# Kernel optimization log

Hardware: AMD Instinct MI355X
Metric: run time of the kernel (lower is better)

The kernel has to match this reference:

```python
import jax, jax.numpy as jnp
import numpy as np

NUM_HEADS = 32
NUM_KV_HEADS = 8
HEAD_DIM = 128
N_REP = NUM_HEADS // NUM_KV_HEADS
ROPE_BASE = 10000.0
NEG_INF = -3.4e38  # large negative for causal mask (matches fp32 min magnitude behavior)


def setup_inputs() -> dict:
    key = jax.random.key(0)
    ks = jax.random.split(key, 5)
    B, S, D = 1, 2048, 4096
    KV = NUM_KV_HEADS * HEAD_DIM  # 1024
    scale = 0.02
    return {
        "hidden_states": jax.random.normal(ks[0], (B, S, D), dtype=jnp.float32),
        "Wq": jax.random.normal(ks[1], (D, D), dtype=jnp.float32) * scale,
        "Wk": jax.random.normal(ks[2], (D, KV), dtype=jnp.float32) * scale,
        "Wv": jax.random.normal(ks[3], (D, KV), dtype=jnp.float32) * scale,
        "Wo": jax.random.normal(ks[4], (D, D), dtype=jnp.float32) * scale,
    }


def _rotate_half(x):
    x1, x2 = jnp.split(x, 2, axis=-1)
    return jnp.concatenate((-x2, x1), axis=-1)


def _rope_cos_sin(B, S, dtype):
    # Qwen/Llama-style rotary embedding, base 10000, position_ids = arange(S)
    inv_freq = 1.0 / (ROPE_BASE ** (jnp.arange(0, HEAD_DIM, 2, dtype=jnp.float32) / HEAD_DIM))
    pos = jnp.arange(S, dtype=jnp.float32)[None, :]            # [1, S] (broadcast over batch)
    freqs = pos[..., None] * inv_freq[None, None, :]           # [1, S, D/2]
    emb = jnp.concatenate((freqs, freqs), axis=-1)             # [1, S, D]
    return jnp.cos(emb).astype(dtype), jnp.sin(emb).astype(dtype)


def reference(hidden_states, Wq, Wk, Wv, Wo):
    B, S, D = hidden_states.shape
    dtype = hidden_states.dtype

    q = (hidden_states @ Wq).reshape(B, S, NUM_HEADS, HEAD_DIM).transpose(0, 2, 1, 3)      # [B,H,S,d]
    k = (hidden_states @ Wk).reshape(B, S, NUM_KV_HEADS, HEAD_DIM).transpose(0, 2, 1, 3)   # [B,Hkv,S,d]
    v = (hidden_states @ Wv).reshape(B, S, NUM_KV_HEADS, HEAD_DIM).transpose(0, 2, 1, 3)

    cos, sin = _rope_cos_sin(B, S, dtype)
    cos = cos[:, None, :, :]  # unsqueeze head dim
    sin = sin[:, None, :, :]
    q = q * cos + _rotate_half(q) * sin
    k = k * cos + _rotate_half(k) * sin

    # repeat_kv: [B,Hkv,S,d] -> [B,H,S,d]
    k = jnp.repeat(k, N_REP, axis=1)
    v = jnp.repeat(v, N_REP, axis=1)

    attn = jnp.einsum("bhqd,bhkd->bhqk", q, k) / jnp.sqrt(jnp.asarray(HEAD_DIM, dtype))
    causal = jnp.where(jnp.arange(S)[:, None] >= jnp.arange(S)[None, :], 0.0, NEG_INF).astype(dtype)
    attn = attn + causal[None, None, :, :]
    attn = jax.nn.softmax(attn.astype(jnp.float32), axis=-1).astype(dtype)

    out = jnp.einsum("bhqk,bhkd->bhqd", attn, v)           # [B,H,S,d]
    out = out.transpose(0, 2, 1, 3).reshape(B, S, NUM_HEADS * HEAD_DIM)
    return out @ Wo
```

## Files before the change

kernel.cpp:

```cpp
#include <hip/hip_runtime.h>
#include <stdint.h>

typedef float f32x4 __attribute__((ext_vector_type(4)));
typedef __bf16 bf16x8 __attribute__((ext_vector_type(8)));
typedef unsigned short u16;
typedef unsigned short u16x8 __attribute__((ext_vector_type(8)));

__device__ __forceinline__ u16 f2b(float f) {
    union { float f; unsigned u; } v; v.f = f;
    return (u16)((v.u + 0x7fffu + ((v.u >> 16) & 1u)) >> 16);
}
__device__ __forceinline__ float b2f(u16 b) {
    union { unsigned u; float f; } v; v.u = ((unsigned)b) << 16;
    return v.f;
}

__device__ __forceinline__ void gload16(const u16* g, u16* s) {
    __builtin_amdgcn_global_load_lds((const __attribute__((address_space(1))) void*)g,
                                     (__attribute__((address_space(3))) void*)s, 16, 0, 0);
}

__global__ __launch_bounds__(256) void k_cast(const float* __restrict__ src, u16* __restrict__ dst, int n) {
    int i = (blockIdx.x * 256 + threadIdx.x) * 8;
    if (i >= n) return;
    const float4* s = (const float4*)(src + i);
    float4 a = s[0], b = s[1];
    u16x8 o;
    o[0] = f2b(a.x); o[1] = f2b(a.y); o[2] = f2b(a.z); o[3] = f2b(a.w);
    o[4] = f2b(b.x); o[5] = f2b(b.y); o[6] = f2b(b.z); o[7] = f2b(b.w);
    *(u16x8*)(dst + i) = o;
}

__global__ __launch_bounds__(256) void k_transpose(const float* __restrict__ src, u16* __restrict__ dst,
                                                   int R, int C) {
    __shared__ float tile[64][65];
    int c0 = blockIdx.x * 64, r0 = blockIdx.y * 64;
    int tx = threadIdx.x & 63, ty = threadIdx.x >> 6;
    #pragma unroll
    for (int r = ty; r < 64; r += 4)
        tile[r][tx] = src[(size_t)(r0 + r) * C + (c0 + tx)];
    __syncthreads();
    #pragma unroll
    for (int r = ty; r < 64; r += 4)
        dst[(size_t)(c0 + r) * R + (r0 + tx)] = f2b(tile[tx][r]);
}

__global__ __launch_bounds__(256) void k_vt(const u16* __restrict__ QKV, u16* __restrict__ VT) {
    __shared__ u16 tile[64][66];
    int kh = blockIdx.z;
    int s0 = blockIdx.y * 64;
    int d0 = blockIdx.x * 64;
    int tx = threadIdx.x & 63, ty = threadIdx.x >> 6;
    #pragma unroll
    for (int r = ty; r < 64; r += 4)
        tile[r][tx] = QKV[(size_t)(s0 + r) * 6144 + 5120 + kh * 128 + d0 + tx];
    __syncthreads();
    #pragma unroll
    for (int r = ty; r < 64; r += 4)
        VT[(size_t)kh * 262144 + (size_t)(d0 + r) * 2048 + s0 + tx] = tile[tx][r];
}

#define STAGE_A(h) do { \
    _Pragma("unroll") for (int i_ = 0; i_ < MFR / 4; ++i_) \
        gload16(gA + (size_t)((h) * (MFR * 16) + i_ * 8) * K + kn, &Ah[nb][h][w * (MFR * 2) + i_ * 8][0]); \
} while (0)
#define STAGE_B1(h) gload16(gB + (size_t)((h) * 64) * K + kn, &Bh[nb][h][w * 8][0])
#define STAGE_ALL do { \
    _Pragma("unroll") for (int h_ = 0; h_ < 2; ++h_) STAGE_A(h_); \
    _Pragma("unroll") for (int h_ = 0; h_ < NFR; ++h_) STAGE_B1(h_); } while (0)
#define RD_AF(MH, AF) do { \
    _Pragma("unroll") for (int mm = 0; mm < MFR / 2; ++mm) \
    _Pragma("unroll") for (int x = 0; x < 2; ++x) \
        AF[mm][x] = *(const bf16x8*)&Ah[c][wm][((MH) * (MFR / 2) + mm) * 16 + lr][(x * 32 + lk) ^ swz]; } while (0)
#define RD_BF1(NF) do { \
    int bc_ = wn * (NFR * 16) + (NF) * 16; \
    _Pragma("unroll") for (int x = 0; x < 2; ++x) \
        bfr[NF][x] = *(const bf16x8*)&Bh[c][bc_ >> 6][(bc_ & 63) + lr][(x * 32 + lk) ^ swz]; } while (0)
#define MMAH(MH, NF, AF) do { \
    _Pragma("unroll") for (int x = 0; x < 2; ++x) \
    _Pragma("unroll") for (int mm = 0; mm < MFR / 2; ++mm) \
        acc[(MH) * (MFR / 2) + mm][NF] = __builtin_amdgcn_mfma_f32_16x16x32_bf16( \
            AF[mm][x], bfr[NF][x], acc[(MH) * (MFR / 2) + mm][NF], 0, 0, 0); } while (0)

template <int MFR, int NFR, typename OutT>
__device__ __forceinline__ void gemm_core(const u16* __restrict__ A, const u16* __restrict__ Bt,
                                          OutT* __restrict__ C, int K, int ldc, int m0, int n0) {
    __shared__ u16 Ah[2][2][MFR * 16][64];
    __shared__ u16 Bh[2][NFR][64][64];
    constexpr int LPT = MFR / 2 + NFR;
    int tid = threadIdx.x;
    int l = tid & 63, w = tid >> 6;
    int wm = w >> 2, wn = w & 3;
    int lr = l & 15, lg = l >> 4, lk = lg * 8;
    int swz = (lr & 7) << 3;
    int srow8 = l >> 3;
    int scol = ((l & 7) ^ srow8) * 8;
    const u16* gA = A  + (size_t)(m0 + w * (MFR * 2) + srow8) * K + scol;
    const u16* gB = Bt + (size_t)(n0 + w * 8 + srow8) * K + scol;
    f32x4 acc[MFR][NFR] = {};
    int NT = K >> 6;

    {
        int kn = 0, nb = 0;
        STAGE_ALL;
    }

    #pragma unroll 2
    for (int t = 0; t < NT; ++t) {
        int c = t & 1, nb = c ^ 1;
        int kn = (t + 1) << 6;
        bool last = (t == NT - 1);
        bf16x8 af0[MFR / 2][2], af1[MFR / 2][2], bfr[NFR][2];
        if (!last) {
            STAGE_ALL;
            asm volatile("s_waitcnt vmcnt(%0)" :: "n"(LPT) : "memory");
        } else {
            asm volatile("s_waitcnt vmcnt(0)" ::: "memory");
        }
        __builtin_amdgcn_s_barrier();
        RD_AF(0, af0);
        #pragma unroll
        for (int nf = 0; nf < NFR; ++nf) {
            RD_BF1(nf);
            __builtin_amdgcn_s_setprio(1);
            MMAH(0, nf, af0);
            __builtin_amdgcn_s_setprio(0);
        }
        RD_AF(1, af1);
        __builtin_amdgcn_s_setprio(1);
        #pragma unroll
        for (int nf = 0; nf < NFR; ++nf)
            MMAH(1, nf, af1);
        __builtin_amdgcn_s_setprio(0);
        __builtin_amdgcn_s_barrier();
    }

    #pragma unroll
    for (int m = 0; m < MFR; ++m)
        #pragma unroll
        for (int n = 0; n < NFR; ++n)
            #pragma unroll
            for (int e = 0; e < 4; ++e) {
                int row = m0 + wm * (MFR * 16) + m * 16 + lg * 4 + e;
                int col = n0 + wn * (NFR * 16) + n * 16 + lr;
                if constexpr (sizeof(OutT) == 4)
                    C[(size_t)row * ldc + col] = acc[m][n][e];
                else
                    C[(size_t)row * ldc + col] = f2b(acc[m][n][e]);
            }
}

__global__ __launch_bounds__(512, 2) void k_gemm_qkv(const u16* __restrict__ hsb,
        const u16* __restrict__ WqkvT, u16* __restrict__ QKVb) {
    int bid = blockIdx.x;
    int ord = (bid & 7) * 32 + (bid >> 3);
    int mt = ord >> 5, nt = ord & 31;
    gemm_core<8, 3, u16>(hsb, WqkvT, QKVb, 4096, 6144, mt * 256, nt * 192);
}

__global__ __launch_bounds__(512, 2) void k_gemm_out(const u16* __restrict__ Ob, const u16* __restrict__ WoT,
                                                     float* __restrict__ out) {
    int bid = blockIdx.x;
    int ord = (bid & 7) * 32 + (bid >> 3);
    int mt = ord >> 4, nt = ord & 15;
    gemm_core<4, 4, float>(Ob, WoT, out, 4096, 4096, mt * 128, nt * 256);
}

__global__ __launch_bounds__(256) void k_rope(u16* __restrict__ QKV) {
    int t = blockIdx.x * 256 + threadIdx.x;
    int i = t & 63;
    int rest = t >> 6;
    int head = rest % 40;
    int s = rest / 40;
    if (s >= 2048) return;
    u16* base = (head < 32) ? (QKV + (size_t)s * 6144 + head * 128)
                            : (QKV + (size_t)s * 6144 + 4096 + (head - 32) * 128);
    float inv = exp2f((float)i * (-13.287712379549449f / 64.0f));
    float fr = (float)s * inv;
    float sn, cs;
    sincosf(fr, &sn, &cs);
    float x1 = b2f(base[i]), x2 = b2f(base[i + 64]);
    base[i]      = f2b(x1 * cs - x2 * sn);
    base[i + 64] = f2b(x2 * cs + x1 * sn);
}

__global__ __launch_bounds__(256, 2) void k_attn(const u16* __restrict__ QKV,
                                                 const u16* __restrict__ VT, u16* __restrict__ O) {
    __shared__ u16 Kl[2][64][128];
    __shared__ u16 VTl[128][64];
    __shared__ u16 Pl[4][32][68];
    int bid = blockIdx.x;
    int kh = bid & 7;
    int x = bid >> 3;
    int j = x >> 2;
    int h = kh * 4 + (x & 3);
    int qb = (j < 8) ? j : 23 - j;
    int q0 = qb * 128;
    int t = threadIdx.x, l = t & 63, w = t >> 6;
    int lr = l & 15, lg = l >> 4;
    const float cexp = 0.12751742f;
    const u16* Kh = QKV + 4096 + kh * 128;
    const u16* VTh = VT + (size_t)kh * 262144;

#define ATT_STAGE_K(B, KV0) do { \
    _Pragma("unroll") for (int i_ = 0; i_ < 4; ++i_) { \
        int r0_ = w * 16 + i_ * 4; \
        int row_ = r0_ + (l >> 4); \
        gload16(Kh + (size_t)((KV0) + row_) * 6144 + ((l & 15) ^ (row_ & 7)) * 8, \
                &Kl[B][r0_][0]); \
    } } while (0)
#define ATT_STAGE_V(KV0) do { \
    _Pragma("unroll") for (int i_ = 0; i_ < 4; ++i_) { \
        int r0_ = w * 32 + i_ * 8; \
        int row_ = r0_ + (l >> 3); \
        gload16(VTh + (size_t)row_ * 2048 + (KV0) + ((l & 7) ^ (row_ & 7)) * 8, \
                &VTl[r0_][0]); \
    } } while (0)

    bf16x8 qf[2][4];
    #pragma unroll
    for (int rb = 0; rb < 2; ++rb) {
        size_t qoff = (size_t)(q0 + w * 32 + rb * 16 + lr) * 6144 + h * 128 + lg * 8;
        #pragma unroll
        for (int d = 0; d < 4; ++d)
            qf[rb][d] = *(const bf16x8*)(QKV + qoff + d * 32);
    }
    bf16x8 ones;
    #pragma unroll
    for (int i = 0; i < 8; ++i) ones[i] = (__bf16)1.0f;

    f32x4 oacc[2][8] = {};
    f32x4 osum[2] = {};
    float mrow[2][4];
    #pragma unroll
    for (int rb = 0; rb < 2; ++rb)
        #pragma unroll
        for (int e = 0; e < 4; ++e) mrow[rb][e] = -3.0e38f;

    int ntiles = 2 * qb + 2;
    int rowmax = q0 + w * 32 + 31;

    ATT_STAGE_K(0, 0);

    for (int kt = 0; kt < ntiles; ++kt) {
        int ck = kt & 1;
        int kv0 = kt * 64;
        bool compute = (kv0 <= rowmax);
        bool more = (kt + 1 < ntiles);
        asm volatile("s_waitcnt vmcnt(0)" ::: "memory");
        __builtin_amdgcn_s_barrier();
        ATT_STAGE_V(kv0);
        if (more) ATT_STAGE_K(ck ^ 1, kv0 + 64);
        __builtin_amdgcn_sched_barrier(0);

        f32x4 sacc[2][4] = {};
        if (compute) {
            #pragma unroll
            for (int d = 0; d < 4; ++d) {
                bf16x8 kf[4];
                #pragma unroll
                for (int cb = 0; cb < 4; ++cb)
                    kf[cb] = *(const bf16x8*)&Kl[ck][cb * 16 + lr][((d * 4 + lg) ^ (lr & 7)) * 8];
                #pragma unroll
                for (int cb = 0; cb < 4; ++cb) {
                    sacc[0][cb] = __builtin_amdgcn_mfma_f32_16x16x32_bf16(qf[0][d], kf[cb], sacc[0][cb], 0, 0, 0);
                    sacc[1][cb] = __builtin_amdgcn_mfma_f32_16x16x32_bf16(qf[1][d], kf[cb], sacc[1][cb], 0, 0, 0);
                }
            }
            if (kt >= 2 * qb) {
                #pragma unroll
                for (int rb = 0; rb < 2; ++rb)
                    #pragma unroll
                    for (int cb = 0; cb < 4; ++cb)
                        #pragma unroll
                        for (int e = 0; e < 4; ++e) {
                            int row = q0 + w * 32 + rb * 16 + lg * 4 + e;
                            int col = kv0 + cb * 16 + lr;
                            if (col > row) sacc[rb][cb][e] = -3.0e38f;
                        }
            }
            float vmax[2][4];
            bool need = false;
            #pragma unroll
            for (int rb = 0; rb < 2; ++rb)
                #pragma unroll
                for (int e = 0; e < 4; ++e) {
                    float v = fmaxf(fmaxf(sacc[rb][0][e], sacc[rb][1][e]), fmaxf(sacc[rb][2][e], sacc[rb][3][e]));
                    v = fmaxf(v, __shfl_xor(v, 1));
                    v = fmaxf(v, __shfl_xor(v, 2));
                    v = fmaxf(v, __shfl_xor(v, 4));
                    v = fmaxf(v, __shfl_xor(v, 8));
                    vmax[rb][e] = v;
                    need = need || (v > mrow[rb][e] + 62.0f);
                }
            if (__any(need)) {
                #pragma unroll
                for (int rb = 0; rb < 2; ++rb)
                    #pragma unroll
                    for (int e = 0; e < 4; ++e) {
                        float mnew = fmaxf(mrow[rb][e], vmax[rb][e]);
                        float alpha = exp2f((mrow[rb][e] - mnew) * cexp);
                        mrow[rb][e] = mnew;
                        osum[rb][e] *= alpha;
                        #pragma unroll
                        for (int db = 0; db < 8; ++db) oacc[rb][db][e] *= alpha;
                    }
            }
            #pragma unroll
            for (int rb = 0; rb < 2; ++rb)
                #pragma unroll
                for (int cb = 0; cb < 4; ++cb)
                    #pragma unroll
                    for (int e = 0; e < 4; ++e)
                        Pl[w][rb * 16 + lg * 4 + e][cb * 16 + lr] =
                            f2b(exp2f((sacc[rb][cb][e] - mrow[rb][e]) * cexp));
        }
        if (more) asm volatile("s_waitcnt vmcnt(4)" ::: "memory");
        else      asm volatile("s_waitcnt vmcnt(0)" ::: "memory");
        __builtin_amdgcn_s_barrier();
        if (compute) {
            asm volatile("s_waitcnt lgkmcnt(0)" ::: "memory");
            __builtin_amdgcn_sched_barrier(0);
            __builtin_amdgcn_s_setprio(1);
            #pragma unroll
            for (int ks = 0; ks < 2; ++ks) {
                bf16x8 pf0 = *(const bf16x8*)&Pl[w][lr][ks * 32 + lg * 8];
                bf16x8 pf1 = *(const bf16x8*)&Pl[w][16 + lr][ks * 32 + lg * 8];
                osum[0] = __builtin_amdgcn_mfma_f32_16x16x32_bf16(pf0, ones, osum[0], 0, 0, 0);
                osum[1] = __builtin_amdgcn_mfma_f32_16x16x32_bf16(pf1, ones, osum[1], 0, 0, 0);
                #pragma unroll
                for (int db = 0; db < 8; ++db) {
                    bf16x8 vf = *(const bf16x8*)&VTl[db * 16 + lr][((ks * 4 + lg) ^ (lr & 7)) * 8];
                    oacc[0][db] = __builtin_amdgcn_mfma_f32_16x16x32_bf16(pf0, vf, oacc[0][db], 0, 0, 0);
                    oacc[1][db] = __builtin_amdgcn_mfma_f32_16x16x32_bf16(pf1, vf, oacc[1][db], 0, 0, 0);
                }
            }
            __builtin_amdgcn_s_setprio(0);
        }
    }
    #pragma unroll
    for (int rb = 0; rb < 2; ++rb)
        #pragma unroll
        for (int db = 0; db < 8; ++db)
            #pragma unroll
            for (int e = 0; e < 4; ++e) {
                int row = q0 + w * 32 + rb * 16 + lg * 4 + e;
                O[(size_t)row * 4096 + h * 128 + db * 16 + lr] = f2b(oacc[rb][db][e] / osum[rb][e]);
            }
#undef ATT_STAGE_K
#undef ATT_STAGE_V
}

extern "C" void kernel_launch(void* const* d_in, const int* in_sizes, int n_in,
                              void* d_out, int out_size, void* d_ws, size_t ws_size,
                              hipStream_t stream) {
    const float* hs = (const float*)d_in[0];
    const float* Wq = (const float*)d_in[1];
    const float* Wk = (const float*)d_in[2];
    const float* Wv = (const float*)d_in[3];
    const float* Wo = (const float*)d_in[4];
    float* out = (float*)d_out;
    char* ws = (char*)d_ws;
    u16* hsb   = (u16*)(ws);
    u16* WqkvT = (u16*)(ws + 16777216);
    u16* QKVb  = (u16*)(ws + 67108864);

    k_cast<<<4096, 256, 0, stream>>>(hs, hsb, 2048 * 4096);
    k_transpose<<<dim3(64, 64), 256, 0, stream>>>(Wq, WqkvT, 4096, 4096);
    k_transpose<<<dim3(16, 64), 256, 0, stream>>>(Wk, WqkvT + (size_t)4096 * 4096, 4096, 1024);
    k_transpose<<<dim3(16, 64), 256, 0, stream>>>(Wv, WqkvT + (size_t)5120 * 4096, 4096, 1024);
    k_gemm_qkv<<<256, 512, 0, stream>>>(hsb, WqkvT, QKVb);
    k_rope<<<20480, 256, 0, stream>>>(QKVb);
    u16* VTb = WqkvT;
    k_vt<<<dim3(2, 32, 8), 256, 0, stream>>>(QKVb, VTb);
    u16* WoT = WqkvT + (size_t)2097152;
    k_transpose<<<dim3(64, 64), 256, 0, stream>>>(Wo, WoT, 4096, 4096);
    u16* Ob = hsb;
    k_attn<<<512, 256, 0, stream>>>(QKVb, VTb, Ob);
    k_gemm_out<<<256, 512, 0, stream>>>(Ob, WoT, out);
}
```

Before: 371.6 us.

## Double-buffer V tiles and split P staging per row-block with swizzled layout

V^T tiles in LDS are now double-buffered and prefetched one iteration ahead together with K, which removes the mid-iteration wait and barrier before the PV product. The P buffer is reduced to 16 rows per wave with an XOR-swizzled layout and is reused for the two row-blocks in turn. The first block's PV MFMAs are interleaved with the second block's exp and store, and the V fragments are kept in registers so the second block reuses them. LDS use goes up for V, which may affect occupancy, and holding V fragments in registers raises register pressure.

```diff
diff --git a/kernel.cpp b/kernel.cpp
--- a/kernel.cpp
+++ b/kernel.cpp
@@ -187,8 +187,8 @@
 __global__ __launch_bounds__(256, 2) void k_attn(const u16* __restrict__ QKV,
                                                  const u16* __restrict__ VT, u16* __restrict__ O) {
     __shared__ u16 Kl[2][64][128];
-    __shared__ u16 VTl[128][64];
-    __shared__ u16 Pl[4][32][68];
+    __shared__ u16 VTl[2][128][64];
+    __shared__ u16 Pl[4][16][64];
     int bid = blockIdx.x;
     int kh = bid & 7;
     int x = bid >> 3;
@@ -209,12 +209,12 @@
         gload16(Kh + (size_t)((KV0) + row_) * 6144 + ((l & 15) ^ (row_ & 7)) * 8, \
                 &Kl[B][r0_][0]); \
     } } while (0)
-#define ATT_STAGE_V(KV0) do { \
+#define ATT_STAGE_V(B, KV0) do { \
     _Pragma("unroll") for (int i_ = 0; i_ < 4; ++i_) { \
         int r0_ = w * 32 + i_ * 8; \
         int row_ = r0_ + (l >> 3); \
         gload16(VTh + (size_t)row_ * 2048 + (KV0) + ((l & 7) ^ (row_ & 7)) * 8, \
-                &VTl[r0_][0]); \
+                &VTl[B][r0_][0]); \
     } } while (0)
 
     bf16x8 qf[2][4];
@@ -241,6 +241,7 @@
     int rowmax = q0 + w * 32 + 31;
 
     ATT_STAGE_K(0, 0);
+    ATT_STAGE_V(0, 0);
 
     for (int kt = 0; kt < ntiles; ++kt) {
         int ck = kt & 1;
@@ -249,12 +250,14 @@
         bool more = (kt + 1 < ntiles);
         asm volatile("s_waitcnt vmcnt(0)" ::: "memory");
         __builtin_amdgcn_s_barrier();
-        ATT_STAGE_V(kv0);
-        if (more) ATT_STAGE_K(ck ^ 1, kv0 + 64);
+        if (more) {
+            ATT_STAGE_V(ck ^ 1, kv0 + 64);
+            ATT_STAGE_K(ck ^ 1, kv0 + 64);
+        }
         __builtin_amdgcn_sched_barrier(0);
 
-        f32x4 sacc[2][4] = {};
         if (compute) {
+            f32x4 sacc[2][4] = {};
             #pragma unroll
             for (int d = 0; d < 4; ++d) {
                 bf16x8 kf[4];
@@ -307,33 +310,56 @@
                     }
             }
             #pragma unroll
-            for (int rb = 0; rb < 2; ++rb)
-                #pragma unroll
-                for (int cb = 0; cb < 4; ++cb)
-                    #pragma unroll
-                    for (int e = 0; e < 4; ++e)
-                        Pl[w][rb * 16 + lg * 4 + e][cb * 16 + lr] =
-                            f2b(exp2f((sacc[rb][cb][e] - mrow[rb][e]) * cexp));
-        }
-        if (more) asm volatile("s_waitcnt vmcnt(4)" ::: "memory");
-        else      asm volatile("s_waitcnt vmcnt(0)" ::: "memory");
-        __builtin_amdgcn_s_barrier();
-        if (compute) {
+            for (int cb = 0; cb < 4; ++cb)
+                #pragma unroll
+                for (int e = 0; e < 4; ++e) {
+                    int row = lg * 4 + e;
+                    int ch = (cb * 2 + (lr >> 3)) ^ (row & 7);
+                    Pl[w][row][ch * 8 + (lr & 7)] =
+                        f2b(exp2f((sacc[0][cb][e] - mrow[0][e]) * cexp));
+                }
             asm volatile("s_waitcnt lgkmcnt(0)" ::: "memory");
             __builtin_amdgcn_sched_barrier(0);
+            bf16x8 pf00 = *(const bf16x8*)&Pl[w][lr][((0 * 4 + lg) ^ (lr & 7)) * 8];
+            bf16x8 pf01 = *(const bf16x8*)&Pl[w][lr][((1 * 4 + lg) ^ (lr & 7)) * 8];
+            asm volatile("s_waitcnt lgkmcnt(0)" ::: "memory");
+            __builtin_amdgcn_sched_barrier(0);
+            #pragma unroll
+            for (int cb = 0; cb < 4; ++cb)
+                #pragma unroll
+                for (int e = 0; e < 4; ++e) {
+                    int row = lg * 4 + e;
+                    int ch = (cb * 2 + (lr >> 3)) ^ (row & 7);
+                    Pl[w][row][ch * 8 + (lr & 7)] =
+                        f2b(exp2f((sacc[1][cb][e] - mrow[1][e]) * cexp));
+                }
+            bf16x8 vfr[2][8];
             __builtin_amdgcn_s_setprio(1);
+            osum[0] = __builtin_amdgcn_mfma_f32_16x16x32_bf16(pf00, ones, osum[0], 0, 0, 0);
+            osum[0] = __builtin_amdgcn_mfma_f32_16x16x32_bf16(pf01, ones, osum[0], 0, 0, 0);
             #pragma unroll
             for (int ks = 0; ks < 2; ++ks) {
-                bf16x8 pf0 = *(const bf16x8*)&Pl[w][lr][ks * 32 + lg * 8];
-                bf16x8 pf1 = *(const bf16x8*)&Pl[w][16 + lr][ks * 32 + lg * 8];
-                osum[0] = __builtin_amdgcn_mfma_f32_16x16x32_bf16(pf0, ones, osum[0], 0, 0, 0);
-                osum[1] = __builtin_amdgcn_mfma_f32_16x16x32_bf16(pf1, ones, osum[1], 0, 0, 0);
+                bf16x8 pf0 = ks ? pf01 : pf00;
                 #pragma unroll
                 for (int db = 0; db < 8; ++db) {
-                    bf16x8 vf = *(const bf16x8*)&VTl[db * 16 + lr][((ks * 4 + lg) ^ (lr & 7)) * 8];
-                    oacc[0][db] = __builtin_amdgcn_mfma_f32_16x16x32_bf16(pf0, vf, oacc[0][db], 0, 0, 0);
-                    oacc[1][db] = __builtin_amdgcn_mfma_f32_16x16x32_bf16(pf1, vf, oacc[1][db], 0, 0, 0);
+                    vfr[ks][db] = *(const bf16x8*)&VTl[ck][db * 16 + lr][((ks * 4 + lg) ^ (lr & 7)) * 8];
+                    oacc[0][db] = __builtin_amdgcn_mfma_f32_16x16x32_bf16(pf0, vfr[ks][db], oacc[0][db], 0, 0, 0);
                 }
+            }
+            __builtin_amdgcn_s_setprio(0);
+            asm volatile("s_waitcnt lgkmcnt(0)" ::: "memory");
+            __builtin_amdgcn_sched_barrier(0);
+            bf16x8 pf10 = *(const bf16x8*)&Pl[w][lr][((0 * 4 + lg) ^ (lr & 7)) * 8];
+            bf16x8 pf11 = *(const bf16x8*)&Pl[w][lr][((1 * 4 + lg) ^ (lr & 7)) * 8];
+            __builtin_amdgcn_s_setprio(1);
+            osum[1] = __builtin_amdgcn_mfma_f32_16x16x32_bf16(pf10, ones, osum[1], 0, 0, 0);
+            osum[1] = __builtin_amdgcn_mfma_f32_16x16x32_bf16(pf11, ones, osum[1], 0, 0, 0);
+            #pragma unroll
+            for (int ks = 0; ks < 2; ++ks) {
+                bf16x8 pf1 = ks ? pf11 : pf10;
+                #pragma unroll
+                for (int db = 0; db < 8; ++db)
+                    oacc[1][db] = __builtin_amdgcn_mfma_f32_16x16x32_bf16(pf1, vfr[ks][db], oacc[1][db], 0, 0, 0);
             }
             __builtin_amdgcn_s_setprio(0);
         }
```

Measured after the change: 375.8 us. About the same (+1.1%).

## Fuse Q RoPE into attention Q load and pack transpose stores

Applied to the files above, without the earlier changes.

Applies rotary embedding to Q inside the attention kernel right after Q fragments are loaded, so the standalone rope pass only touches the K heads (a fifth of the heads). This removes a global read/write pass over the Q part of the QKV buffer. The weight transpose kernel now writes two bf16 values per 32-bit store instead of one 16-bit store. The cost is extra sincos work per attention block, recomputed for each head sharing a position, and reads from the transpose tile that are no longer padded for that access pattern.

```diff
diff --git a/kernel.cpp b/kernel.cpp
--- a/kernel.cpp
+++ b/kernel.cpp
@@ -40,9 +40,12 @@
     for (int r = ty; r < 64; r += 4)
         tile[r][tx] = src[(size_t)(r0 + r) * C + (c0 + tx)];
     __syncthreads();
-    #pragma unroll
-    for (int r = ty; r < 64; r += 4)
-        dst[(size_t)(c0 + r) * R + (r0 + tx)] = f2b(tile[tx][r]);
+    int hx = threadIdx.x & 31, ty8 = threadIdx.x >> 5;
+    #pragma unroll
+    for (int r = ty8; r < 64; r += 8) {
+        unsigned v = (unsigned)f2b(tile[hx * 2][r]) | ((unsigned)f2b(tile[hx * 2 + 1][r]) << 16);
+        *(unsigned*)&dst[(size_t)(c0 + r) * R + (r0 + hx * 2)] = v;
+    }
 }
 
 __global__ __launch_bounds__(256) void k_vt(const u16* __restrict__ QKV, u16* __restrict__ VT) {
@@ -166,15 +169,14 @@
     gemm_core<4, 4, float>(Ob, WoT, out, 4096, 4096, mt * 128, nt * 256);
 }
 
-__global__ __launch_bounds__(256) void k_rope(u16* __restrict__ QKV) {
+__global__ __launch_bounds__(256) void k_rope_k(u16* __restrict__ QKV) {
     int t = blockIdx.x * 256 + threadIdx.x;
     int i = t & 63;
     int rest = t >> 6;
-    int head = rest % 40;
-    int s = rest / 40;
+    int head = rest & 7;
+    int s = rest >> 3;
     if (s >= 2048) return;
-    u16* base = (head < 32) ? (QKV + (size_t)s * 6144 + head * 128)
-                            : (QKV + (size_t)s * 6144 + 4096 + (head - 32) * 128);
+    u16* base = QKV + (size_t)s * 6144 + 4096 + head * 128;
     float inv = exp2f((float)i * (-13.287712379549449f / 64.0f));
     float fr = (float)s * inv;
     float sn, cs;
@@ -225,6 +227,27 @@
         for (int d = 0; d < 4; ++d)
             qf[rb][d] = *(const bf16x8*)(QKV + qoff + d * 32);
     }
+    #pragma unroll
+    for (int rb = 0; rb < 2; ++rb) {
+        int s = q0 + w * 32 + rb * 16 + lr;
+        #pragma unroll
+        for (int d2 = 0; d2 < 2; ++d2) {
+            u16x8 lo = (u16x8)qf[rb][d2], hi = (u16x8)qf[rb][d2 + 2];
+            #pragma unroll
+            for (int jj = 0; jj < 8; ++jj) {
+                int i = d2 * 32 + lg * 8 + jj;
+                float inv = exp2f((float)i * (-13.287712379549449f / 64.0f));
+                float fr = (float)s * inv;
+                float sn, cs;
+                sincosf(fr, &sn, &cs);
+                float x1 = b2f(lo[jj]), x2 = b2f(hi[jj]);
+                lo[jj] = f2b(x1 * cs - x2 * sn);
+                hi[jj] = f2b(x2 * cs + x1 * sn);
+            }
+            qf[rb][d2] = (bf16x8)lo;
+            qf[rb][d2 + 2] = (bf16x8)hi;
+        }
+    }
     bf16x8 ones;
     #pragma unroll
     for (int i = 0; i < 8; ++i) ones[i] = (__bf16)1.0f;
@@ -370,7 +393,7 @@
     k_transpose<<<dim3(16, 64), 256, 0, stream>>>(Wk, WqkvT + (size_t)4096 * 4096, 4096, 1024);
     k_transpose<<<dim3(16, 64), 256, 0, stream>>>(Wv, WqkvT + (size_t)5120 * 4096, 4096, 1024);
     k_gemm_qkv<<<256, 512, 0, stream>>>(hsb, WqkvT, QKVb);
-    k_rope<<<20480, 256, 0, stream>>>(QKVb);
+    k_rope_k<<<4096, 256, 0, stream>>>(QKVb);
     u16* VTb = WqkvT;
     k_vt<<<dim3(2, 32, 8), 256, 0, stream>>>(QKVb, VTb);
     u16* WoT = WqkvT + (size_t)2097152;
```

Result: no change. 368.7 us (-0.8%).
